# Kernel tuning notes

Hardware: AMD Instinct MI355X
Metric: run time of the kernel (lower is better)

Reference implementation:

```python
import jax, jax.numpy as jnp
import numpy as np

N_HEADS = 8
WINDOW = 4
KS = 3
N_LAYERS = 6
EPS = 1e-5


def _rel_to_abs(x):
    # x: [B,H,L,2L-1] relative logits -> [B,H,L,L] absolute
    b, h, l, _ = x.shape
    x = jnp.pad(x, ((0, 0), (0, 0), (0, 0), (0, 1)))
    x = x.reshape(b, h, l * 2 * l)
    x = jnp.pad(x, ((0, 0), (0, 0), (0, l - 1)))
    return x.reshape(b, h, l + 1, 2 * l - 1)[:, :, :l, l - 1:]


def _abs_to_rel(x):
    # x: [B,H,L,L] -> [B,H,L,2L-1]
    b, h, l, _ = x.shape
    x = jnp.pad(x, ((0, 0), (0, 0), (0, 0), (0, l - 1)))
    x = x.reshape(b, h, l * (2 * l - 1))
    x = jnp.pad(x, ((0, 0), (0, 0), (l, 0)))
    return x.reshape(b, h, l, 2 * l)[:, :, :, 1:]


def _get_rel_emb(emb, t):
    # emb: [2*WINDOW+1, D] -> [2t-1, D]
    pad = max(t - (WINDOW + 1), 0)
    start = max((WINDOW + 1) - t, 0)
    emb = jnp.pad(emb, ((pad, pad), (0, 0)))
    return emb[start:start + 2 * t - 1]


def _layer_norm(x, g, b):
    # normalize over channel dim (axis 1) of [B,C,T]
    m = jnp.mean(x, axis=1, keepdims=True)
    v = jnp.mean((x - m) ** 2, axis=1, keepdims=True)
    return (x - m) * jax.lax.rsqrt(v + EPS) * g[None, :, None] + b[None, :, None]


def _attn(x, w, bvec, erk, erv, attn_mask):
    # x: [B,C,T]; w: [4,C,C] (q,k,v,o 1x1 convs); bvec: [4,C]
    B, C, T = x.shape
    kch = C // N_HEADS

    def proj(i):
        h = jnp.einsum('oc,bct->bot', w[i], x) + bvec[i][None, :, None]
        return h.reshape(B, N_HEADS, kch, T).transpose(0, 1, 3, 2)  # [B,H,T,D]

    q, k, v = proj(0), proj(1), proj(2)
    scale = np.float32(1.0 / np.sqrt(kch))
    scores = jnp.einsum('bhtd,bhsd->bhts', q * scale, k)
    kr = _get_rel_emb(erk, T)  # [2T-1, D]
    scores = scores + _rel_to_abs(jnp.einsum('bhtd,md->bhtm', q * scale, kr))
    scores = jnp.where(attn_mask == 0, jnp.float32(-1e4), scores)
    p = jax.nn.softmax(scores, axis=-1)
    out = jnp.einsum('bhts,bhsd->bhtd', p, v)
    vr = _get_rel_emb(erv, T)
    out = out + jnp.einsum('bhtm,md->bhtd', _abs_to_rel(p), vr)
    out = out.transpose(0, 1, 3, 2).reshape(B, C, T)
    return jnp.einsum('oc,bct->bot', w[3], out) + bvec[3][None, :, None]


def _conv1d_same(h, wt, bt):
    pad_l, pad_r = (KS - 1) // 2, KS // 2
    hp = jnp.pad(h, ((0, 0), (0, 0), (pad_l, pad_r)))
    y = jax.lax.conv_general_dilated(hp, wt, (1,), 'VALID',
                                     dimension_numbers=('NCH', 'OIH', 'NCH'))
    return y + bt[None, :, None]


def _ffn(x, mask, w1, b1, w2, b2):
    h = jax.nn.relu(_conv1d_same(x * mask, w1, b1))  # activation=None -> relu
    return _conv1d_same(h * mask, w2, b2) * mask


def reference(x, x_mask, attn_w, attn_b, erk, erv, ln1_g, ln1_b,
              ffn_w1, ffn_b1, ffn_w2, ffn_b2, ln2_g, ln2_b):
    attn_mask = x_mask[:, :, :, None] * x_mask[:, :, None, :]  # [B,1,T,T]
    x = x * x_mask
    for i in range(N_LAYERS):
        y = _attn(x, attn_w[i], attn_b[i], erk[i], erv[i], attn_mask)
        x = _layer_norm(x + y, ln1_g[i], ln1_b[i])
        y = _ffn(x, x_mask, ffn_w1[i], ffn_b1[i], ffn_w2[i], ffn_b2[i])
        x = _layer_norm(x + y, ln2_g[i], ln2_b[i])
    return x * x_mask


def setup_inputs() -> dict:
    B, C, T, F, L = 8, 512, 1024, 2048, N_LAYERS
    kch = C // N_HEADS
    key = jax.random.key(0)
    ks = jax.random.split(key, 8)
    std = 0.02
    return {
        'x': jax.random.normal(ks[0], (B, C, T), jnp.float32),
        'x_mask': jnp.ones((B, 1, T), jnp.float32),
        'attn_w': jax.random.normal(ks[1], (L, 4, C, C), jnp.float32) * std,
        'attn_b': jnp.zeros((L, 4, C), jnp.float32),
        'erk': jax.random.normal(ks[2], (L, 2 * WINDOW + 1, kch), jnp.float32) * (kch ** -0.5),
        'erv': jax.random.normal(ks[3], (L, 2 * WINDOW + 1, kch), jnp.float32) * (kch ** -0.5),
        'ln1_g': jnp.ones((L, C), jnp.float32),
        'ln1_b': jnp.zeros((L, C), jnp.float32),
        'ffn_w1': jax.random.normal(ks[4], (L, F, C, KS), jnp.float32) * std,
        'ffn_b1': jnp.zeros((L, F), jnp.float32),
        'ffn_w2': jax.random.normal(ks[5], (L, C, F, KS), jnp.float32) * std,
        'ffn_b2': jnp.zeros((L, C), jnp.float32),
        'ln2_g': jnp.ones((L, C), jnp.float32),
        'ln2_b': jnp.zeros((L, C), jnp.float32),
    }
```

## Files before the change

### kernel.cpp

```cpp
#include <hip/hip_runtime.h>

typedef __bf16 bf16_t;
typedef __bf16 bf16x8 __attribute__((ext_vector_type(8)));
typedef __bf16 bf16x4 __attribute__((ext_vector_type(4)));
typedef float  f32x4  __attribute__((ext_vector_type(4)));

#define AS1 __attribute__((address_space(1)))
#define AS3 __attribute__((address_space(3)))

#define CMAX 16.0f

template<int BM, int BN, int OUTMN, int CONV, int BIAS, int RELU, int MASK>
__global__ __launch_bounds__(256)
void gemm_nt(const bf16_t* __restrict__ A, const bf16_t* __restrict__ B,
             bf16_t* __restrict__ C, const float* __restrict__ bias,
             const float* __restrict__ mask, const bf16_t* __restrict__ zpage,
             int K, int lda, int ldb, int ldc, int CIN,
             long sAb, long sAh, long sBb, long sBh, long sCb, long sCh)
{
    constexpr int BK = 32;
    __shared__ bf16_t As[BM * BK];
    __shared__ bf16_t Bs[BN * BK];
    const int z = blockIdx.z;
    int tap0 = 0;
    if constexpr (CONV == 2) {
        tap0 = z;
        A += (long)tap0 * CIN;
    } else {
        A += (long)(z >> 3) * sAb + (long)(z & 7) * sAh;
        B += (long)(z >> 3) * sBb + (long)(z & 7) * sBh;
        C += (long)(z >> 3) * sCb + (long)(z & 7) * sCh;
    }
    const int m0 = blockIdx.y * BM;
    const int n0 = blockIdx.x * BN;
    const int tid = threadIdx.x;
    const int wid = tid >> 6, lane = tid & 63;
    constexpr int WM = BM / 2, WN = BN / 2;
    constexpr int FM = WM / 16, FN = WN / 16;
    const int wm = wid >> 1, wn = wid & 1;

    f32x4 acc[FM][FN] = {};

    constexpr int ACH = BM / 64;
    constexpr int BCH = BN / 64;
    const int rquad = lane >> 2;
    const int koff  = (lane & 3) * 8;

    int tap = 0, cc0 = 0;
    for (int k0 = 0; k0 < K; k0 += BK) {
        #pragma unroll
        for (int q = 0; q < ACH; ++q) {
            int ch  = wid * ACH + q;
            int row = ch * 16 + rquad;
            const bf16_t* src = A + (long)(m0 + row) * lda + (k0 + koff);
            __builtin_amdgcn_global_load_lds((const AS1 void*)src,
                                             (AS3 void*)(As + ch * 512), 16, 0, 0);
        }
        #pragma unroll
        for (int q = 0; q < BCH; ++q) {
            int ch  = wid * BCH + q;
            int row = ch * 16 + rquad;
            const bf16_t* src;
            if constexpr (CONV == 1) {
                int tl = (n0 & 1023) + row + tap - 1;
                src = ((unsigned)tl < 1024u)
                    ? B + (long)(n0 + row + tap - 1) * ldb + (cc0 + koff)
                    : zpage + koff;
            } else if constexpr (CONV == 2) {
                int tl = (n0 & 1023) + row + tap0 - 1;
                src = ((unsigned)tl < 1024u)
                    ? B + (long)(n0 + row + tap0 - 1) * ldb + (k0 + koff)
                    : zpage + koff;
            } else {
                src = B + (long)(n0 + row) * ldb + (k0 + koff);
            }
            __builtin_amdgcn_global_load_lds((const AS1 void*)src,
                                             (AS3 void*)(Bs + ch * 512), 16, 0, 0);
        }
        if constexpr (CONV == 1) { cc0 += BK; if (cc0 == CIN) { cc0 = 0; ++tap; } }
        __syncthreads();

        const bf16_t* Ab = As + (wm * WM + (lane & 15)) * BK + ((lane >> 4) * 8);
        const bf16_t* Bb = Bs + (wn * WN + (lane & 15)) * BK + ((lane >> 4) * 8);
        bf16x8 af[FM], bv[FN];
        #pragma unroll
        for (int i = 0; i < FM; ++i) af[i] = *(const bf16x8*)(Ab + i * 16 * BK);
        #pragma unroll
        for (int j = 0; j < FN; ++j) bv[j] = *(const bf16x8*)(Bb + j * 16 * BK);
        #pragma unroll
        for (int i = 0; i < FM; ++i)
            #pragma unroll
            for (int j = 0; j < FN; ++j)
                acc[i][j] = __builtin_amdgcn_mfma_f32_16x16x32_bf16(af[i], bv[j], acc[i][j], 0, 0, 0);
        __syncthreads();
    }

    const int mw = m0 + wm * WM, nw = n0 + wn * WN;
    #pragma unroll
    for (int i = 0; i < FM; ++i) {
        const int mb = mw + i * 16 + (lane >> 4) * 4;
        f32x4 bvv = {};
        if constexpr (BIAS) bvv = *(const f32x4*)(bias + mb);
        #pragma unroll
        for (int j = 0; j < FN; ++j) {
            const int nn = nw + j * 16 + (lane & 15);
            f32x4 v = acc[i][j];
            if constexpr (BIAS) v += bvv;
            if constexpr (RELU) {
                #pragma unroll
                for (int r = 0; r < 4; ++r) v[r] = fmaxf(v[r], 0.f);
            }
            if constexpr (MASK) v *= mask[nn];
            bf16x4 o;
            #pragma unroll
            for (int r = 0; r < 4; ++r) o[r] = (bf16_t)v[r];
            if constexpr (CONV == 2) {
                *(bf16x4*)(C + ((long)tap0 << 22) + (long)nn * 512 + mb) = o;
            } else if constexpr (OUTMN) {
                #pragma unroll
                for (int r = 0; r < 4; ++r) C[(long)(mb + r) * ldc + nn] = (bf16_t)v[r];
            } else {
                *(bf16x4*)(C + (long)nn * ldc + mb) = o;
            }
        }
    }
}

__global__ __launch_bounds__(256)
void rel_qk_mfma(const bf16_t* __restrict__ qk, const float* __restrict__ erk_l,
                 float* __restrict__ R)
{
    const int w = threadIdx.x >> 6, lane = threadIdx.x & 63;
    const int hi = lane >> 4, li = lane & 15;
    const int bh = blockIdx.x, b = bh >> 3, h = bh & 7;
    const int t0 = blockIdx.y * 64 + w * 16;
    const long nb = (long)b * 1024;

    const bf16_t* qrow = qk + (nb + t0 + li) * 1024 + h * 64 + hi * 8;
    bf16x8 aq0 = *(const bf16x8*)(qrow);
    bf16x8 aq1 = *(const bf16x8*)(qrow + 32);

    bf16x8 be0, be1;
    #pragma unroll
    for (int e = 0; e < 8; ++e) {
        float v0 = (li < 9) ? erk_l[li * 64 + hi * 8 + e] : 0.f;
        float v1 = (li < 9) ? erk_l[li * 64 + 32 + hi * 8 + e] : 0.f;
        be0[e] = (bf16_t)v0; be1[e] = (bf16_t)v1;
    }
    f32x4 acc = {};
    acc = __builtin_amdgcn_mfma_f32_16x16x32_bf16(aq0, be0, acc, 0, 0, 0);
    acc = __builtin_amdgcn_mfma_f32_16x16x32_bf16(aq1, be1, acc, 0, 0, 0);
    if (li < 9) {
        #pragma unroll
        for (int r = 0; r < 4; ++r) {
            int t = t0 + hi * 4 + r;
            R[((long)bh * 1024 + t) * 9 + li] = acc[r];
        }
    }
}

__global__ __launch_bounds__(256)
void mask_bias(const float* __restrict__ mask, float* __restrict__ kb)
{
    int i = blockIdx.x * 256 + threadIdx.x;
    if (i < 8192) kb[i] = (mask[i] == 0.f) ? -1e4f : 0.f;
}

__global__ __launch_bounds__(256)
void flash_attn(const bf16_t* __restrict__ qk, const bf16_t* __restrict__ vt,
                const float* __restrict__ R, const float* __restrict__ kb,
                bf16_t* __restrict__ out, float* __restrict__ lsum,
                float* __restrict__ pband)
{
    __shared__ bf16_t P_lds[4 * 1024];
    const int w = threadIdx.x >> 6, lane = threadIdx.x & 63;
    const int hi = lane >> 4, li = lane & 15;
    const int bh = blockIdx.x, b = bh >> 3, h = bh & 7;
    const int q0 = blockIdx.y * 64 + w * 16;
    const long nbase = (long)b * 1024;
    char* pw = (char*)(P_lds + w * 1024);

    const bf16_t* qrow = qk + (nbase + q0 + li) * 1024 + h * 64 + hi * 8;
    bf16x8 aq0 = *(const bf16x8*)(qrow);
    bf16x8 aq1 = *(const bf16x8*)(qrow + 32);

    bf16x8 ones;
    #pragma unroll
    for (int e = 0; e < 8; ++e) ones[e] = (bf16_t)1.0f;

    f32x4 acc_o[4] = {};
    f32x4 acc_l = {};

    const bf16_t* kbase = qk + nbase * 1024 + 512 + h * 64 + hi * 8;
    const bf16_t* vbase = vt + (long)(h * 64 + li) * 8192 + nbase + hi * 8;
    const float* kbp = kb + b * 1024;

    bf16x8 kc[4][2], vv[4][2];
    #pragma unroll
    for (int j = 0; j < 4; ++j) {
        const bf16_t* kr = kbase + (long)(j * 16 + li) * 1024;
        kc[j][0] = *(const bf16x8*)kr;
        kc[j][1] = *(const bf16x8*)(kr + 32);
    }

    for (int it = 0; it < 16; ++it) {
        const int s0 = it * 64;
        #pragma unroll
        for (int j2 = 0; j2 < 4; ++j2) {
            const bf16_t* vr = vbase + (long)(j2 * 16) * 8192 + s0;
            vv[j2][0] = *(const bf16x8*)vr;
            vv[j2][1] = *(const bf16x8*)(vr + 32);
        }
        float kbv[4];
        #pragma unroll
        for (int j = 0; j < 4; ++j) kbv[j] = kbp[s0 + j * 16 + li];
        f32x4 sc[4];
        __builtin_amdgcn_s_setprio(1);
        #pragma unroll
        for (int j = 0; j < 4; ++j) {
            f32x4 a = {};
            a = __builtin_amdgcn_mfma_f32_16x16x32_bf16(aq0, kc[j][0], a, 0, 0, 0);
            a = __builtin_amdgcn_mfma_f32_16x16x32_bf16(aq1, kc[j][1], a, 0, 0, 0);
            sc[j] = a;
        }
        __builtin_amdgcn_s_setprio(0);
        const int s1 = (s0 + 64) & 1023;
        #pragma unroll
        for (int j = 0; j < 4; ++j) {
            const bf16_t* kr = kbase + (long)(s1 + j * 16 + li) * 1024;
            kc[j][0] = *(const bf16x8*)kr;
            kc[j][1] = *(const bf16x8*)(kr + 32);
        }
        #pragma unroll
        for (int j = 0; j < 4; ++j) {
            const int sb = s0 + j * 16;
            const bool near = (sb + 15 >= q0 - 4) && (sb <= q0 + 19);
            const int s_abs = sb + li;
            #pragma unroll
            for (int r = 0; r < 4; ++r) {
                const int q_abs = q0 + hi * 4 + r;
                float v = sc[j][r] + kbv[j];
                if (near) {
                    int jb = s_abs - q_abs + 4;
                    if ((unsigned)jb < 9u)
                        v += R[((long)bh * 1024 + q_abs) * 9 + jb];
                }
                float pex = __expf(v - CMAX);
                sc[j][r] = pex;
                if (near) {
                    int jb = s_abs - q_abs + 4;
                    if ((unsigned)jb < 9u)
                        pband[((long)bh * 1024 + q_abs) * 9 + jb] = pex;
                }
            }
        }
        #pragma unroll
        for (int j = 0; j < 4; ++j)
            #pragma unroll
            for (int r = 0; r < 4; ++r) {
                int q = hi * 4 + r;
                int c = (j * 32 + li * 2) ^ ((q & 7) << 4);
                *(bf16_t*)(pw + q * 128 + c) = (bf16_t)sc[j][r];
            }
        asm volatile("s_waitcnt lgkmcnt(0)" ::: "memory");
        __builtin_amdgcn_s_setprio(1);
        #pragma unroll
        for (int half = 0; half < 2; ++half) {
            int cr = (half * 64 + hi * 16) ^ ((li & 7) << 4);
            bf16x8 pa = *(const bf16x8*)(pw + li * 128 + cr);
            #pragma unroll
            for (int j2 = 0; j2 < 4; ++j2)
                acc_o[j2] = __builtin_amdgcn_mfma_f32_16x16x32_bf16(pa, vv[j2][half], acc_o[j2], 0, 0, 0);
            acc_l = __builtin_amdgcn_mfma_f32_16x16x32_bf16(pa, ones, acc_l, 0, 0, 0);
        }
        __builtin_amdgcn_s_setprio(0);
    }

    #pragma unroll
    for (int r = 0; r < 4; ++r) {
        const float inv = 1.f / acc_l[r];
        const int q_abs = q0 + hi * 4 + r;
        #pragma unroll
        for (int j2 = 0; j2 < 4; ++j2) {
            const int d = j2 * 16 + li;
            out[(nbase + q_abs) * 512 + h * 64 + d] = (bf16_t)(acc_o[j2][r] * inv);
        }
        if (li == 0) lsum[(long)bh * 1024 + q_abs] = acc_l[r];
    }
}

__global__ __launch_bounds__(256)
void band_apply(const float* __restrict__ pband, const float* __restrict__ lsum,
                const float* __restrict__ erv_l, bf16_t* __restrict__ out)
{
    int gw = blockIdx.x * 4 + (threadIdx.x >> 6);
    int bh = gw >> 10, t = gw & 1023;
    int b = bh >> 3, h = bh & 7;
    int lane = threadIdx.x & 63;
    float invl = 1.f / lsum[gw];
    const float* pb = pband + (long)gw * 9;
    float acc = 0.f;
    #pragma unroll
    for (int j = 0; j < 9; ++j) {
        int s = t + j - 4;
        if ((unsigned)s < 1024u)
            acc += pb[j] * erv_l[j * 64 + lane];
    }
    long oidx = ((long)b * 1024 + t) * 512 + h * 64 + lane;
    out[oidx] = (bf16_t)((float)out[oidx] + acc * invl);
}

template<int MASKOUT>
__global__ __launch_bounds__(256)
void ln_residual(float* __restrict__ xres, const bf16_t* __restrict__ y,
                 bf16_t* __restrict__ xbf, const float* __restrict__ g,
                 const float* __restrict__ bvec, const float* __restrict__ mask)
{
    int gw = blockIdx.x * 4 + (threadIdx.x >> 6);
    int lane = threadIdx.x & 63;
    long base = (long)gw * 512 + lane * 8;
    f32x4 x0 = *(const f32x4*)(xres + base);
    f32x4 x1 = *(const f32x4*)(xres + base + 4);
    bf16x8 yv = *(const bf16x8*)(y + base);
    float s[8];
    #pragma unroll
    for (int e = 0; e < 4; ++e) { s[e] = x0[e] + (float)yv[e]; s[4 + e] = x1[e] + (float)yv[4 + e]; }
    float sum = 0.f, sq = 0.f;
    #pragma unroll
    for (int e = 0; e < 8; ++e) { sum += s[e]; sq += s[e] * s[e]; }
    #pragma unroll
    for (int o = 1; o < 64; o <<= 1) { sum += __shfl_xor(sum, o); sq += __shfl_xor(sq, o); }
    float mean = sum * (1.f / 512.f);
    float var  = sq * (1.f / 512.f) - mean * mean;
    float rstd = rsqrtf(var + 1e-5f);
    f32x4 g0 = *(const f32x4*)(g + lane * 8);
    f32x4 g1 = *(const f32x4*)(g + lane * 8 + 4);
    f32x4 b0 = *(const f32x4*)(bvec + lane * 8);
    f32x4 b1 = *(const f32x4*)(bvec + lane * 8 + 4);
    float mk = MASKOUT ? mask[gw] : 1.f;
    f32x4 o0, o1; bf16x8 ob;
    #pragma unroll
    for (int e = 0; e < 4; ++e) {
        float v0 = (s[e] - mean) * rstd * g0[e] + b0[e];
        float v1 = (s[4 + e] - mean) * rstd * g1[e] + b1[e];
        o0[e] = v0; o1[e] = v1;
        ob[e] = (bf16_t)(v0 * mk); ob[4 + e] = (bf16_t)(v1 * mk);
    }
    *(f32x4*)(xres + base) = o0;
    *(f32x4*)(xres + base + 4) = o1;
    *(bf16x8*)(xbf + base) = ob;
}

__global__ __launch_bounds__(256)
void ln_residual_p3(float* __restrict__ xres, const bf16_t* __restrict__ part,
                    bf16_t* __restrict__ xbf, const float* __restrict__ g,
                    const float* __restrict__ bvec, const float* __restrict__ bias,
                    const float* __restrict__ mask)
{
    int gw = blockIdx.x * 4 + (threadIdx.x >> 6);
    int lane = threadIdx.x & 63;
    long base = (long)gw * 512 + lane * 8;
    bf16x8 pa = *(const bf16x8*)(part + base);
    bf16x8 pbv = *(const bf16x8*)(part + base + (1l << 22));
    bf16x8 pc = *(const bf16x8*)(part + base + (2l << 22));
    f32x4 x0 = *(const f32x4*)(xres + base);
    f32x4 x1 = *(const f32x4*)(xres + base + 4);
    f32x4 bi0 = *(const f32x4*)(bias + lane * 8);
    f32x4 bi1 = *(const f32x4*)(bias + lane * 8 + 4);
    float mk = mask[gw];
    float s[8];
    #pragma unroll
    for (int e = 0; e < 4; ++e) {
        float y0 = ((float)pa[e] + (float)pbv[e] + (float)pc[e] + bi0[e]) * mk;
        float y1 = ((float)pa[4 + e] + (float)pbv[4 + e] + (float)pc[4 + e] + bi1[e]) * mk;
        s[e] = x0[e] + y0; s[4 + e] = x1[e] + y1;
    }
    float sum = 0.f, sq = 0.f;
    #pragma unroll
    for (int e = 0; e < 8; ++e) { sum += s[e]; sq += s[e] * s[e]; }
    #pragma unroll
    for (int o = 1; o < 64; o <<= 1) { sum += __shfl_xor(sum, o); sq += __shfl_xor(sq, o); }
    float mean = sum * (1.f / 512.f);
    float var  = sq * (1.f / 512.f) - mean * mean;
    float rstd = rsqrtf(var + 1e-5f);
    f32x4 g0 = *(const f32x4*)(g + lane * 8);
    f32x4 g1 = *(const f32x4*)(g + lane * 8 + 4);
    f32x4 b0 = *(const f32x4*)(bvec + lane * 8);
    f32x4 b1 = *(const f32x4*)(bvec + lane * 8 + 4);
    f32x4 o0, o1; bf16x8 ob;
    #pragma unroll
    for (int e = 0; e < 4; ++e) {
        float v0 = (s[e] - mean) * rstd * g0[e] + b0[e];
        float v1 = (s[4 + e] - mean) * rstd * g1[e] + b1[e];
        o0[e] = v0; o1[e] = v1;
        ob[e] = (bf16_t)v0; ob[4 + e] = (bf16_t)v1;
    }
    *(f32x4*)(xres + base) = o0;
    *(f32x4*)(xres + base + 4) = o1;
    *(bf16x8*)(xbf + base) = ob;
}

__global__ __launch_bounds__(256)
void transpose_in_k(const float* __restrict__ x, const float* __restrict__ mask,
                    float* __restrict__ xres, bf16_t* __restrict__ xbf)
{
    __shared__ float tile[32][33];
    int b = blockIdx.z, c0 = blockIdx.y * 32, t0 = blockIdx.x * 32;
    int tx = threadIdx.x & 31, ty = threadIdx.x >> 5;
    #pragma unroll
    for (int r = 0; r < 4; ++r) {
        int cl = ty + r * 8;
        tile[cl][tx] = x[((long)b * 512 + c0 + cl) * 1024 + t0 + tx];
    }
    __syncthreads();
    #pragma unroll
    for (int r = 0; r < 4; ++r) {
        int tl = ty + r * 8;
        int n = b * 1024 + t0 + tl;
        float v = tile[tx][tl] * mask[n];
        xres[(long)n * 512 + c0 + tx] = v;
        xbf[(long)n * 512 + c0 + tx] = (bf16_t)v;
    }
}

__global__ __launch_bounds__(256)
void transpose_out_k(const float* __restrict__ xres, const float* __restrict__ mask,
                     float* __restrict__ out)
{
    __shared__ float tile[32][33];
    int b = blockIdx.z, c0 = blockIdx.y * 32, t0 = blockIdx.x * 32;
    int tx = threadIdx.x & 31, ty = threadIdx.x >> 5;
    #pragma unroll
    for (int r = 0; r < 4; ++r) {
        int tl = ty + r * 8;
        int n = b * 1024 + t0 + tl;
        tile[tl][tx] = xres[(long)n * 512 + c0 + tx] * mask[n];
    }
    __syncthreads();
    #pragma unroll
    for (int r = 0; r < 4; ++r) {
        int cl = ty + r * 8;
        out[((long)b * 512 + c0 + cl) * 1024 + t0 + tx] = tile[tx][cl];
    }
}

__global__ __launch_bounds__(256)
void pack_attn_w(const float* __restrict__ w, bf16_t* __restrict__ Wqk,
                 bf16_t* __restrict__ Wv, bf16_t* __restrict__ Wo)
{
    int idx = blockIdx.x * 256 + threadIdx.x;
    if (idx >= 4 * 512 * 512) return;
    int c = idx & 511;
    int o = (idx >> 9) & 511;
    int which = idx >> 18;
    float v = w[idx];
    if (which == 0) v *= 0.125f;
    if (which <= 1)      Wqk[(which * 512 + o) * 512 + c] = (bf16_t)v;
    else if (which == 2) Wv[o * 512 + c] = (bf16_t)v;
    else                 Wo[o * 512 + c] = (bf16_t)v;
}

__global__ __launch_bounds__(256)
void pack_attn_b(const float* __restrict__ bsrc, float* __restrict__ bqk)
{
    int idx = blockIdx.x * 256 + threadIdx.x;
    if (idx >= 6 * 2 * 512) return;
    int c = idx & 511, which = (idx >> 9) & 1, i = idx >> 10;
    float v = bsrc[(i * 4 + which) * 512 + c];
    if (which == 0) v *= 0.125f;
    bqk[i * 1024 + which * 512 + c] = v;
}

__global__ __launch_bounds__(256)
void pack_conv_w(const float* __restrict__ w1, const float* __restrict__ w2,
                 bf16_t* __restrict__ W1p, bf16_t* __restrict__ W2p)
{
    int idx = blockIdx.x * 256 + threadIdx.x;
    if (idx < 2048 * 1536) {
        int c = idx & 511;
        int k = (idx >> 9) % 3;
        int f = idx / 1536;
        W1p[idx] = (bf16_t)w1[(f * 512 + c) * 3 + k];
    } else {
        int j = idx - 2048 * 1536;
        int f = j & 2047;
        int k = (j >> 11) % 3;
        int ci = j / 6144;
        W2p[j] = (bf16_t)w2[ci * 6144 + f * 3 + k];
    }
}

extern "C" void kernel_launch(void* const* d_in, const int* in_sizes, int n_in,
                              void* d_out, int out_size, void* d_ws, size_t ws_size,
                              hipStream_t stream)
{
    const float* x      = (const float*)d_in[0];
    const float* xmask  = (const float*)d_in[1];
    const float* attn_w = (const float*)d_in[2];
    const float* attn_b = (const float*)d_in[3];
    const float* erk    = (const float*)d_in[4];
    const float* erv    = (const float*)d_in[5];
    const float* ln1g   = (const float*)d_in[6];
    const float* ln1b   = (const float*)d_in[7];
    const float* w1     = (const float*)d_in[8];
    const float* b1in   = (const float*)d_in[9];
    const float* w2     = (const float*)d_in[10];
    const float* b2in   = (const float*)d_in[11];
    const float* ln2g   = (const float*)d_in[12];
    const float* ln2b   = (const float*)d_in[13];
    float* out = (float*)d_out;

    char* p = (char*)d_ws;
    auto alloc = [&](size_t bytes) {
        char* r = p;
        p += (bytes + 255) & ~(size_t)255;
        return r;
    };
    bf16_t* zpage = (bf16_t*)alloc(1024);
    bf16_t* Wqk_l = (bf16_t*)alloc(1024l * 512 * 2);
    bf16_t* Wv_l  = (bf16_t*)alloc(512l * 512 * 2);
    bf16_t* Wo_l  = (bf16_t*)alloc(512l * 512 * 2);
    bf16_t* W1p_l = (bf16_t*)alloc(2048l * 1536 * 2);
    bf16_t* W2p_l = (bf16_t*)alloc(512l * 6144 * 2);
    float*  bqk   = (float*)alloc(6l * 1024 * 4);
    float*  xres  = (float*)alloc(8192l * 512 * 4);
    bf16_t* xbf   = (bf16_t*)alloc(8192l * 512 * 2);
    bf16_t* big   = (bf16_t*)alloc(8192l * 2048 * 2);
    bf16_t* ybuf  = (bf16_t*)alloc(8192l * 512 * 2);
    bf16_t* part  = (bf16_t*)alloc(3l * 8192 * 512 * 2);
    float*  R     = (float*)alloc(64l * 1024 * 9 * 4);
    float*  lsum  = (float*)alloc(64l * 1024 * 4);
    float*  pband = (float*)alloc(64l * 1024 * 9 * 4);
    float*  kb    = (float*)alloc(8192l * 4);
    (void)in_sizes; (void)n_in; (void)out_size; (void)ws_size;

    bf16_t* qk       = big;
    bf16_t* vt       = big + 8192l * 1024;
    bf16_t* attn_out = vt + 512l * 8192;
    bf16_t* hbuf     = big;

    hipMemsetAsync(zpage, 0, 1024, stream);
    pack_attn_b<<<24, 256, 0, stream>>>(attn_b, bqk);
    mask_bias<<<32, 256, 0, stream>>>(xmask, kb);
    transpose_in_k<<<dim3(32, 16, 8), 256, 0, stream>>>(x, xmask, xres, xbf);

    for (int i = 0; i < 6; ++i) {
        pack_attn_w<<<4096, 256, 0, stream>>>(attn_w + (long)i * 4 * 512 * 512,
                                              Wqk_l, Wv_l, Wo_l);
        pack_conv_w<<<24576, 256, 0, stream>>>(w1 + (long)i * 2048 * 512 * 3,
                                               w2 + (long)i * 512 * 2048 * 3,
                                               W1p_l, W2p_l);

        gemm_nt<64, 128, 0, 0, 1, 0, 0><<<dim3(64, 16, 1), 256, 0, stream>>>(
            Wqk_l, xbf, qk, bqk + i * 1024, nullptr, zpage,
            512, 512, 512, 1024, 0, 0, 0, 0, 0, 0, 0);
        gemm_nt<64, 64, 1, 0, 1, 0, 0><<<dim3(128, 8, 1), 256, 0, stream>>>(
            Wv_l, xbf, vt, attn_b + (i * 4 + 2) * 512, nullptr, zpage,
            512, 512, 512, 8192, 0, 0, 0, 0, 0, 0, 0);
        rel_qk_mfma<<<dim3(64, 16), 256, 0, stream>>>(qk, erk + i * 576, R);
        flash_attn<<<dim3(64, 16), 256, 0, stream>>>(qk, vt, R, kb,
                                                     attn_out, lsum, pband);
        band_apply<<<16384, 256, 0, stream>>>(pband, lsum, erv + i * 576,
                                              attn_out);
        gemm_nt<64, 64, 0, 0, 1, 0, 0><<<dim3(128, 8, 1), 256, 0, stream>>>(
            Wo_l, attn_out, ybuf, attn_b + (i * 4 + 3) * 512, nullptr, zpage,
            512, 512, 512, 512, 0, 0, 0, 0, 0, 0, 0);
        ln_residual<1><<<2048, 256, 0, stream>>>(xres, ybuf, xbf,
                                                 ln1g + i * 512, ln1b + i * 512, xmask);
        gemm_nt<64, 128, 0, 1, 1, 1, 1><<<dim3(64, 32, 1), 256, 0, stream>>>(
            W1p_l, xbf, hbuf, b1in + i * 2048, xmask, zpage,
            1536, 1536, 512, 2048, 512, 0, 0, 0, 0, 0, 0);
        gemm_nt<64, 128, 0, 2, 0, 0, 0><<<dim3(64, 8, 3), 256, 0, stream>>>(
            W2p_l, hbuf, part, nullptr, nullptr, zpage,
            2048, 6144, 2048, 512, 2048, 0, 0, 0, 0, 0, 0);
        ln_residual_p3<<<2048, 256, 0, stream>>>(xres, part, xbf,
                                                 ln2g + i * 512, ln2b + i * 512,
                                                 b2in + i * 512, xmask);
    }

    transpose_out_k<<<dim3(32, 16, 8), 256, 0, stream>>>(xres, xmask, out);
}
```

Measured before the change: 2.429 ms.

## Fuse relative-key logits and relative-value band into flash attention kernel

Computes the relative-key logits inside flash_attn and keeps them in per-wave shared memory, instead of running a separate rel_qk kernel and reading R from global memory. The banded softmax probabilities also stay in shared memory and are applied against erv in the epilogue, so the band_apply kernel and the R, pband and lsum buffers are removed. This saves two kernel launches per layer and the global traffic between them. In exchange the epilogue does a 9-tap loop per output element and the kernel uses more shared memory.

Result: no change. 2.395 ms (-1.4%).

```diff
diff --git a/kernel.cpp b/kernel.cpp
--- a/kernel.cpp
+++ b/kernel.cpp
@@ -127,39 +127,6 @@
 }
 
 __global__ __launch_bounds__(256)
-void rel_qk_mfma(const bf16_t* __restrict__ qk, const float* __restrict__ erk_l,
-                 float* __restrict__ R)
-{
-    const int w = threadIdx.x >> 6, lane = threadIdx.x & 63;
-    const int hi = lane >> 4, li = lane & 15;
-    const int bh = blockIdx.x, b = bh >> 3, h = bh & 7;
-    const int t0 = blockIdx.y * 64 + w * 16;
-    const long nb = (long)b * 1024;
-
-    const bf16_t* qrow = qk + (nb + t0 + li) * 1024 + h * 64 + hi * 8;
-    bf16x8 aq0 = *(const bf16x8*)(qrow);
-    bf16x8 aq1 = *(const bf16x8*)(qrow + 32);
-
-    bf16x8 be0, be1;
-    #pragma unroll
-    for (int e = 0; e < 8; ++e) {
-        float v0 = (li < 9) ? erk_l[li * 64 + hi * 8 + e] : 0.f;
-        float v1 = (li < 9) ? erk_l[li * 64 + 32 + hi * 8 + e] : 0.f;
-        be0[e] = (bf16_t)v0; be1[e] = (bf16_t)v1;
-    }
-    f32x4 acc = {};
-    acc = __builtin_amdgcn_mfma_f32_16x16x32_bf16(aq0, be0, acc, 0, 0, 0);
-    acc = __builtin_amdgcn_mfma_f32_16x16x32_bf16(aq1, be1, acc, 0, 0, 0);
-    if (li < 9) {
-        #pragma unroll
-        for (int r = 0; r < 4; ++r) {
-            int t = t0 + hi * 4 + r;
-            R[((long)bh * 1024 + t) * 9 + li] = acc[r];
-        }
-    }
-}
-
-__global__ __launch_bounds__(256)
 void mask_bias(const float* __restrict__ mask, float* __restrict__ kb)
 {
     int i = blockIdx.x * 256 + threadIdx.x;
@@ -168,11 +135,12 @@
 
 __global__ __launch_bounds__(256)
 void flash_attn(const bf16_t* __restrict__ qk, const bf16_t* __restrict__ vt,
-                const float* __restrict__ R, const float* __restrict__ kb,
-                bf16_t* __restrict__ out, float* __restrict__ lsum,
-                float* __restrict__ pband)
+                const float* __restrict__ erk_l, const float* __restrict__ kb,
+                const float* __restrict__ erv_l, bf16_t* __restrict__ out)
 {
     __shared__ bf16_t P_lds[4 * 1024];
+    __shared__ float Rw[4][16 * 9];
+    __shared__ float Pw[4][16 * 9];
     const int w = threadIdx.x >> 6, lane = threadIdx.x & 63;
     const int hi = lane >> 4, li = lane & 15;
     const int bh = blockIdx.x, b = bh >> 3, h = bh & 7;
@@ -184,6 +152,24 @@
     bf16x8 aq0 = *(const bf16x8*)(qrow);
     bf16x8 aq1 = *(const bf16x8*)(qrow + 32);
 
+    {
+        bf16x8 be0, be1;
+        #pragma unroll
+        for (int e = 0; e < 8; ++e) {
+            float v0 = (li < 9) ? erk_l[li * 64 + hi * 8 + e] : 0.f;
+            float v1 = (li < 9) ? erk_l[li * 64 + 32 + hi * 8 + e] : 0.f;
+            be0[e] = (bf16_t)v0; be1[e] = (bf16_t)v1;
+        }
+        f32x4 racc = {};
+        racc = __builtin_amdgcn_mfma_f32_16x16x32_bf16(aq0, be0, racc, 0, 0, 0);
+        racc = __builtin_amdgcn_mfma_f32_16x16x32_bf16(aq1, be1, racc, 0, 0, 0);
+        if (li < 9) {
+            #pragma unroll
+            for (int r = 0; r < 4; ++r)
+                Rw[w][(hi * 4 + r) * 9 + li] = racc[r];
+        }
+    }
+
     bf16x8 ones;
     #pragma unroll
     for (int e = 0; e < 8; ++e) ones[e] = (bf16_t)1.0f;
@@ -238,20 +224,19 @@
             const int s_abs = sb + li;
             #pragma unroll
             for (int r = 0; r < 4; ++r) {
-                const int q_abs = q0 + hi * 4 + r;
+                const int row = hi * 4 + r;
+                const int q_abs = q0 + row;
                 float v = sc[j][r] + kbv[j];
+                float pex;
                 if (near) {
                     int jb = s_abs - q_abs + 4;
-                    if ((unsigned)jb < 9u)
-                        v += R[((long)bh * 1024 + q_abs) * 9 + jb];
+                    if ((unsigned)jb < 9u) v += Rw[w][row * 9 + jb];
+                    pex = __expf(v - CMAX);
+                    if ((unsigned)jb < 9u) Pw[w][row * 9 + jb] = pex;
+                } else {
+                    pex = __expf(v - CMAX);
                 }
-                float pex = __expf(v - CMAX);
                 sc[j][r] = pex;
-                if (near) {
-                    int jb = s_abs - q_abs + 4;
-                    if ((unsigned)jb < 9u)
-                        pband[((long)bh * 1024 + q_abs) * 9 + jb] = pex;
-                }
             }
         }
         #pragma unroll
@@ -278,36 +263,20 @@
 
     #pragma unroll
     for (int r = 0; r < 4; ++r) {
+        const int row = hi * 4 + r;
+        const int q_abs = q0 + row;
         const float inv = 1.f / acc_l[r];
-        const int q_abs = q0 + hi * 4 + r;
         #pragma unroll
         for (int j2 = 0; j2 < 4; ++j2) {
             const int d = j2 * 16 + li;
-            out[(nbase + q_abs) * 512 + h * 64 + d] = (bf16_t)(acc_o[j2][r] * inv);
-        }
-        if (li == 0) lsum[(long)bh * 1024 + q_abs] = acc_l[r];
-    }
-}
-
-__global__ __launch_bounds__(256)
-void band_apply(const float* __restrict__ pband, const float* __restrict__ lsum,
-                const float* __restrict__ erv_l, bf16_t* __restrict__ out)
-{
-    int gw = blockIdx.x * 4 + (threadIdx.x >> 6);
-    int bh = gw >> 10, t = gw & 1023;
-    int b = bh >> 3, h = bh & 7;
-    int lane = threadIdx.x & 63;
-    float invl = 1.f / lsum[gw];
-    const float* pb = pband + (long)gw * 9;
-    float acc = 0.f;
-    #pragma unroll
-    for (int j = 0; j < 9; ++j) {
-        int s = t + j - 4;
-        if ((unsigned)s < 1024u)
-            acc += pb[j] * erv_l[j * 64 + lane];
-    }
-    long oidx = ((long)b * 1024 + t) * 512 + h * 64 + lane;
-    out[oidx] = (bf16_t)((float)out[oidx] + acc * invl);
+            float v = acc_o[j2][r];
+            #pragma unroll
+            for (int jb = 0; jb < 9; ++jb)
+                if ((unsigned)(q_abs + jb - 4) < 1024u)
+                    v += Pw[w][row * 9 + jb] * erv_l[jb * 64 + d];
+            out[(nbase + q_abs) * 512 + h * 64 + d] = (bf16_t)(v * inv);
+        }
+    }
 }
 
 template<int MASKOUT>
@@ -528,9 +497,6 @@
     bf16_t* big   = (bf16_t*)alloc(8192l * 2048 * 2);
     bf16_t* ybuf  = (bf16_t*)alloc(8192l * 512 * 2);
     bf16_t* part  = (bf16_t*)alloc(3l * 8192 * 512 * 2);
-    float*  R     = (float*)alloc(64l * 1024 * 9 * 4);
-    float*  lsum  = (float*)alloc(64l * 1024 * 4);
-    float*  pband = (float*)alloc(64l * 1024 * 9 * 4);
     float*  kb    = (float*)alloc(8192l * 4);
     (void)in_sizes; (void)n_in; (void)out_size; (void)ws_size;
 
@@ -557,11 +523,8 @@
         gemm_nt<64, 64, 1, 0, 1, 0, 0><<<dim3(128, 8, 1), 256, 0, stream>>>(
             Wv_l, xbf, vt, attn_b + (i * 4 + 2) * 512, nullptr, zpage,
             512, 512, 512, 8192, 0, 0, 0, 0, 0, 0, 0);
-        rel_qk_mfma<<<dim3(64, 16), 256, 0, stream>>>(qk, erk + i * 576, R);
-        flash_attn<<<dim3(64, 16), 256, 0, stream>>>(qk, vt, R, kb,
-                                                     attn_out, lsum, pband);
-        band_apply<<<16384, 256, 0, stream>>>(pband, lsum, erv + i * 576,
-                                              attn_out);
+        flash_attn<<<dim3(64, 16), 256, 0, stream>>>(qk, vt, erk + i * 576, kb,
+                                                     erv + i * 576, attn_out);
         gemm_nt<64, 64, 0, 0, 1, 0, 0><<<dim3(128, 8, 1), 256, 0, stream>>>(
             Wo_l, attn_out, ybuf, attn_b + (i * 4 + 3) * 512, nullptr, zpage,
             512, 512, 512, 512, 0, 0, 0, 0, 0, 0, 0);
```
